# Kernel tuning notes

Hardware: AMD Instinct MI355X
Metric: run time of the kernel (lower is better)

## Reference

```python
import jax, jax.numpy as jnp
import numpy as np

D_MODEL = 1024
NUM_HEADS = 16
D_K = D_MODEL // NUM_HEADS  # 64


def _xavier(key, shape):
    fan_in, fan_out = shape[-1], shape[-2]
    limit = float(np.sqrt(6.0 / (fan_in + fan_out)))
    return jax.random.uniform(key, shape, jnp.float32, -limit, limit)


def setup_inputs() -> dict:
    key = jax.random.key(0)
    kx, kq, kk, kv, ko = jax.random.split(key, 5)
    x = jax.random.normal(kx, (2, 2048, D_MODEL), dtype=jnp.float32)
    q_heads = _xavier(kq, (NUM_HEADS, D_K, D_MODEL))
    k_heads = _xavier(kk, (NUM_HEADS, D_K, D_MODEL))
    v_heads = _xavier(kv, (NUM_HEADS, D_K, D_MODEL))
    output_proj = _xavier(ko, (D_MODEL, NUM_HEADS * D_K))
    return {"x": x, "q_heads": q_heads, "k_heads": k_heads,
            "v_heads": v_heads, "output_proj": output_proj}


def reference(x, q_heads, k_heads, v_heads, output_proj):
    # x: [b, s, d]; q/k/v_heads: [h, dk, d]; output_proj: [d, h*dk]
    b, s, d = x.shape
    h, dk, _ = q_heads.shape
    scale = 1.0 / jnp.sqrt(jnp.asarray(dk, x.dtype))
    # per-head projections: [b, h, s, dk]
    Q = jnp.einsum('bsd,hkd->bhsk', x, q_heads)
    K = jnp.einsum('bsd,hkd->bhsk', x, k_heads)
    V = jnp.einsum('bsd,hkd->bhsk', x, v_heads)
    scores = jnp.einsum('bhqk,bhsk->bhqs', Q, K) * scale  # [b,h,s,s]
    causal = jnp.tril(jnp.ones((s, s), dtype=bool))       # True where allowed
    scores = jnp.where(causal, scores, -jnp.inf)
    attn = jax.nn.softmax(scores, axis=-1)
    out = jnp.einsum('bhqs,bhsk->bhqk', attn, V)           # [b,h,s,dk]
    out = out.transpose(0, 2, 1, 3).reshape(b, s, h * dk)  # [b,s,h*dk]
    return jnp.einsum('bsk,dk->bsd', out, output_proj)
```

## Files before the change

### kernel.cpp

```cpp
#include <hip/hip_runtime.h>
#include <hip/hip_bf16.h>
#include <math.h>

#define D_MODEL 1024
#define NHEADS  16
#define DK      64
#define SEQ     2048
#define KDIM    1024

typedef __bf16 bf16x8 __attribute__((ext_vector_type(8)));
typedef float  f32x4  __attribute__((ext_vector_type(4)));

__device__ __forceinline__ void gload16(const void* g, void* l) {
    __builtin_amdgcn_global_load_lds(
        (const __attribute__((address_space(1))) void*)g,
        (__attribute__((address_space(3))) void*)l, 16, 0, 0);
}

__device__ __forceinline__ unsigned short f2bf(float f) {
    __hip_bfloat16 h = __float2bfloat16(f);
    return *(unsigned short*)&h;
}

__device__ __forceinline__ unsigned pk2bf(float a, float b) {
    __hip_bfloat162 h = __float22bfloat162_rn(make_float2(a, b));
    return *(unsigned*)&h;
}

#define QSCALE 0.18033688011112042f

__global__ __launch_bounds__(256) void cast_kernel(
    const float* __restrict__ x,
    const float* __restrict__ qw,
    const float* __restrict__ kw,
    const float* __restrict__ vw,
    const float* __restrict__ wo,
    unsigned short* __restrict__ xb,
    unsigned short* __restrict__ wqkv,
    unsigned short* __restrict__ wob)
{
    const size_t t = (size_t)blockIdx.x * 256 + threadIdx.x;
    const size_t X4 = 1048576;
    const size_t W4 = 262144;

    const float* src;
    unsigned short* dst;
    size_t o;
    if (t < X4)            { src = x;  dst = xb;             o = t; }
    else if (t < X4 + W4)  { src = qw; dst = wqkv;           o = t - X4; }
    else if (t < X4 + 2*W4){ src = kw; dst = wqkv + 1048576; o = t - X4 - W4; }
    else if (t < X4 + 3*W4){ src = vw; dst = wqkv + 2097152; o = t - X4 - 2*W4; }
    else                   { src = wo; dst = wob;            o = t - X4 - 3*W4; }

    float4 v = ((const float4*)src)[o];
    ushort4 r;
    r.x = f2bf(v.x); r.y = f2bf(v.y); r.z = f2bf(v.z); r.w = f2bf(v.w);
    ((ushort4*)dst)[o] = r;
}

template<int MODE>
__global__ __launch_bounds__(256) void mfma_gemm(
    const unsigned short* __restrict__ A,
    const unsigned short* __restrict__ B,
    float* __restrict__ C0,
    unsigned short* __restrict__ Qb,
    unsigned short* __restrict__ Kb,
    unsigned short* __restrict__ Vtb)
{
    __shared__ __align__(16) unsigned short smem[16384];
    unsigned short* As = smem;
    unsigned short* Bs = smem + 4096;

    const int tid  = threadIdx.x;
    const int wave = tid >> 6;
    const int lane = tid & 63;
    const int wr   = wave >> 1;
    const int wc   = wave & 1;
    const int quad = lane >> 4;
    const int l16  = lane & 15;

    const int rowBase = blockIdx.y * 128;
    const int colBase = blockIdx.x * 128;

    f32x4 acc[4][4];
    const f32x4 z = {0.f, 0.f, 0.f, 0.f};
#pragma unroll
    for (int i = 0; i < 4; ++i)
#pragma unroll
        for (int j = 0; j < 4; ++j) acc[i][j] = z;

    const int srow = lane >> 2;
    const int skof = (lane & 3) * 8;

    for (int k0 = 0; k0 < KDIM; k0 += 32) {
        __syncthreads();

        const unsigned short* ga =
            A + (size_t)(rowBase + wave * 32) * KDIM + k0;
        gload16(ga + (size_t)srow * KDIM + skof,        &As[(wave*32)    * 32]);
        gload16(ga + (size_t)(16 + srow) * KDIM + skof, &As[(wave*32+16) * 32]);

        const unsigned short* gb =
            B + (size_t)(colBase + wave * 32) * KDIM + k0;
        gload16(gb + (size_t)srow * KDIM + skof,        &Bs[(wave*32)    * 32]);
        gload16(gb + (size_t)(16 + srow) * KDIM + skof, &Bs[(wave*32+16) * 32]);

        __syncthreads();

        bf16x8 af[4], bfr[4];
#pragma unroll
        for (int t = 0; t < 4; ++t)
            af[t] = *(const bf16x8*)&As[(wr*64 + t*16 + l16) * 32 + quad*8];
#pragma unroll
        for (int t = 0; t < 4; ++t)
            bfr[t] = *(const bf16x8*)&Bs[(wc*64 + t*16 + l16) * 32 + quad*8];

#pragma unroll
        for (int tr = 0; tr < 4; ++tr)
#pragma unroll
            for (int tc = 0; tc < 4; ++tc)
                acc[tr][tc] = __builtin_amdgcn_mfma_f32_16x16x32_bf16(
                    af[tr], bfr[tc], acc[tr][tc], 0, 0, 0);
    }

    if (MODE == 0) {
        const int mat = colBase >> 10;
        const int b   = rowBase >> 11;
        const int sblk = rowBase & (SEQ - 1);
        if (mat == 2) {
#pragma unroll
            for (int tr = 0; tr < 4; ++tr) {
#pragma unroll
                for (int tc = 0; tc < 4; ++tc) {
                    const int s0 = sblk + wr*64 + tr*16 + quad*4;
                    const int kk = (colBase & 1023) + wc*64 + tc*16 + l16;
                    const int h  = kk >> 6, dk = kk & 63;
                    ushort4 pk;
                    pk.x = f2bf(acc[tr][tc][0]); pk.y = f2bf(acc[tr][tc][1]);
                    pk.z = f2bf(acc[tr][tc][2]); pk.w = f2bf(acc[tr][tc][3]);
                    *(ushort4*)(Vtb + ((size_t)(b*NHEADS + h)*DK + dk)*SEQ + s0) = pk;
                }
            }
        } else {
            const float sc = (mat == 0) ? QSCALE : 1.0f;
            __syncthreads();
#pragma unroll
            for (int tr = 0; tr < 4; ++tr) {
#pragma unroll
                for (int tc = 0; tc < 4; ++tc) {
                    const int col   = wc*64 + tc*16 + l16;
                    const int cbase = col >> 3, c7 = col & 7;
#pragma unroll
                    for (int reg = 0; reg < 4; ++reg) {
                        const int row = wr*64 + tr*16 + quad*4 + reg;
                        const int chunk = cbase ^ (row & 15);
                        smem[row*128 + chunk*8 + c7] = f2bf(acc[tr][tc][reg] * sc);
                    }
                }
            }
            __syncthreads();
            const int h0 = (colBase & 1023) >> 6;
            unsigned short* dstb = (mat == 0) ? Qb : Kb;
#pragma unroll
            for (int i = 0; i < 8; ++i) {
                const int g    = i*256 + tid;
                const int head = g >> 10;
                const int s    = (g >> 3) & 127;
                const int ci   = g & 7;
                const int chunk = (head*8 + ci) ^ (s & 15);
                uint4 v = *(uint4*)&smem[s*128 + chunk*8];
                *(uint4*)(dstb + ((size_t)(b*NHEADS + h0 + head)*SEQ + sblk + s)*DK
                               + ci*8) = v;
            }
        }
    } else {
#pragma unroll
        for (int tr = 0; tr < 4; ++tr) {
#pragma unroll
            for (int tc = 0; tc < 4; ++tc) {
                const int grow0 = rowBase + wr*64 + tr*16 + quad*4;
                const int gcol  = colBase + wc*64 + tc*16 + l16;
#pragma unroll
                for (int reg = 0; reg < 4; ++reg)
                    C0[(size_t)(grow0 + reg) * D_MODEL + gcol] = acc[tr][tc][reg];
            }
        }
    }
}

__global__ __launch_bounds__(256) void attn_mfma_kernel(
    const unsigned short* __restrict__ Qb,
    const unsigned short* __restrict__ Kb,
    const unsigned short* __restrict__ Vtb,
    unsigned short* __restrict__ O)
{
    __shared__ unsigned short Ks[64 * 64];
    __shared__ unsigned short Vs[64 * 64];
    __shared__ unsigned short Ps[4 * 16 * 64];

    const int bh   = blockIdx.x;
    const int qt   = 31 - blockIdx.y;
    const int wave = threadIdx.x >> 6;
    const int lane = threadIdx.x & 63;
    const int quad = lane >> 4;
    const int l16  = lane & 15;

    const size_t qrow = (size_t)bh * SEQ + qt*64 + wave*16 + l16;
    bf16x8 aq0 = *(const bf16x8*)(Qb + qrow * DK + quad*8);
    bf16x8 aq1 = *(const bf16x8*)(Qb + qrow * DK + 32 + quad*8);

    f32x4 o_acc[4];
    const f32x4 z = {0.f, 0.f, 0.f, 0.f};
#pragma unroll
    for (int i = 0; i < 4; ++i) o_acc[i] = z;
    float lrow = 0.f;

    const int srow8  = lane >> 3;
    const int schunk = lane & 7;
    const unsigned short* Kbase = Kb  + (size_t)bh * SEQ * DK;
    const unsigned short* Vbase = Vtb + (size_t)bh * DK * SEQ;
    unsigned short* Pw = &Ps[wave * 1024];

    const int ntiles = qt + 1;
    for (int jt = 0; jt < ntiles; ++jt) {
        const int j0 = jt * 64;
        __syncthreads();
#pragma unroll
        for (int n = 0; n < 2; ++n) {
            const int r = wave*16 + n*8 + srow8;
            gload16(Kbase + (size_t)(j0 + r) * DK + (schunk ^ srow8) * 8,
                    &Ks[(wave*16 + n*8) * 64]);
            gload16(Vbase + (size_t)r * SEQ + j0 + (schunk ^ srow8) * 8,
                    &Vs[(wave*16 + n*8) * 64]);
        }
        __syncthreads();

        f32x4 st[4];
#pragma unroll
        for (int ct = 0; ct < 4; ++ct) {
            const int r = ct*16 + l16;
            bf16x8 k0 = *(const bf16x8*)&Ks[r*64 + ((quad     ^ (r&7)) * 8)];
            bf16x8 k1 = *(const bf16x8*)&Ks[r*64 + (((4+quad) ^ (r&7)) * 8)];
            f32x4 t = z;
            t = __builtin_amdgcn_mfma_f32_16x16x32_bf16(k0, aq0, t, 0, 0, 0);
            t = __builtin_amdgcn_mfma_f32_16x16x32_bf16(k1, aq1, t, 0, 0, 0);
            st[ct] = t;
        }

        if (jt == qt) {
#pragma unroll
            for (int ct = 0; ct < 4; ++ct)
#pragma unroll
                for (int reg = 0; reg < 4; ++reg) {
                    const int kl = ct*16 + quad*4 + reg;
                    const int ql = wave*16 + l16;
                    if (kl > ql) st[ct][reg] = -1e30f;
                }
        }

        float rs = 0.f;
#pragma unroll
        for (int ct = 0; ct < 4; ++ct)
#pragma unroll
            for (int reg = 0; reg < 4; ++reg) {
                float p = exp2f(st[ct][reg]);
                st[ct][reg] = p;
                rs += p;
            }
        rs += __shfl_xor(rs, 16);
        rs += __shfl_xor(rs, 32);
        lrow += rs;

#pragma unroll
        for (int ct = 0; ct < 4; ++ct) {
            uint2 pk;
            pk.x = pk2bf(st[ct][0], st[ct][1]);
            pk.y = pk2bf(st[ct][2], st[ct][3]);
            const int g = (ct*4 + quad) ^ ((l16 & 7) << 1);
            *(uint2*)(Pw + l16*64 + g*4) = pk;
        }

        bf16x8 bp0 = *(const bf16x8*)(Pw + l16*64 + ((quad     ^ (l16&7)) * 8));
        bf16x8 bp1 = *(const bf16x8*)(Pw + l16*64 + (((4+quad) ^ (l16&7)) * 8));

#pragma unroll
        for (int ot = 0; ot < 4; ++ot) {
            const int r = ot*16 + l16;
            bf16x8 v0 = *(const bf16x8*)&Vs[r*64 + ((quad     ^ (r&7)) * 8)];
            bf16x8 v1 = *(const bf16x8*)&Vs[r*64 + (((4+quad) ^ (r&7)) * 8)];
            o_acc[ot] = __builtin_amdgcn_mfma_f32_16x16x32_bf16(v0, bp0, o_acc[ot], 0, 0, 0);
            o_acc[ot] = __builtin_amdgcn_mfma_f32_16x16x32_bf16(v1, bp1, o_acc[ot], 0, 0, 0);
        }
    }

    const float inv = 1.f / lrow;
    const int b = bh >> 4, h = bh & 15;
    const int sg = qt*64 + wave*16 + l16;
    unsigned short* orow = O + ((size_t)(b * SEQ + sg)) * D_MODEL + h * DK;
#pragma unroll
    for (int ot = 0; ot < 4; ++ot) {
        uint2 pk;
        pk.x = pk2bf(o_acc[ot][0] * inv, o_acc[ot][1] * inv);
        pk.y = pk2bf(o_acc[ot][2] * inv, o_acc[ot][3] * inv);
        *(uint2*)(orow + ot*16 + quad*4) = pk;
    }
}

extern "C" void kernel_launch(void* const* d_in, const int* in_sizes, int n_in,
                              void* d_out, int out_size, void* d_ws, size_t ws_size,
                              hipStream_t stream) {
    const float* x  = (const float*)d_in[0];
    const float* qw = (const float*)d_in[1];
    const float* kw = (const float*)d_in[2];
    const float* vw = (const float*)d_in[3];
    const float* wo = (const float*)d_in[4];
    float* out = (float*)d_out;

    char* ws = (char*)d_ws;
    unsigned short* Qb   = (unsigned short*)(ws);
    unsigned short* Kb   = (unsigned short*)(ws + (size_t) 8*1024*1024);
    unsigned short* Vtb  = (unsigned short*)(ws + (size_t)16*1024*1024);
    unsigned short* AO   = (unsigned short*)(ws + (size_t)24*1024*1024);
    unsigned short* XB   = (unsigned short*)(ws + (size_t)32*1024*1024);
    unsigned short* WQKV = (unsigned short*)(ws + (size_t)40*1024*1024);
    unsigned short* WOB  = (unsigned short*)(ws + (size_t)46*1024*1024);

    cast_kernel<<<8192, 256, 0, stream>>>(x, qw, kw, vw, wo, XB, WQKV, WOB);

    dim3 g1(24, 32);
    mfma_gemm<0><<<g1, 256, 0, stream>>>(XB, WQKV, nullptr, Qb, Kb, Vtb);

    dim3 g2(32, 32);
    attn_mfma_kernel<<<g2, 256, 0, stream>>>(Qb, Kb, Vtb, AO);

    dim3 g3(8, 32);
    mfma_gemm<1><<<g3, 256, 0, stream>>>(AO, WOB, out, nullptr, nullptr, nullptr);
}
```

Baseline: 187.5 us.

## Feed P to PV MFMA from registers and retile output projection GEMM

In the attention kernel, the softmax probabilities are no longer staged through per-wave shared memory. They are packed straight into register fragments for the 16x16x16 bf16 MFMA variant, with V read in matching 4-element chunks. This removes LDS writes and reads of P, but doubles the MFMA instruction count and adds more, smaller V loads. Separately, the output projection moves to its own GEMM kernel with 64x128 tiles, doubling the grid to 512 blocks for better CU occupancy on a small GEMM.

```diff
diff --git a/kernel.cpp b/kernel.cpp
--- a/kernel.cpp
+++ b/kernel.cpp
@@ -9,6 +9,7 @@
 #define KDIM    1024
 
 typedef __bf16 bf16x8 __attribute__((ext_vector_type(8)));
+typedef short  s16x4  __attribute__((ext_vector_type(4)));
 typedef float  f32x4  __attribute__((ext_vector_type(4)));
 
 __device__ __forceinline__ void gload16(const void* g, void* l) {
@@ -58,11 +59,9 @@
     ((ushort4*)dst)[o] = r;
 }
 
-template<int MODE>
-__global__ __launch_bounds__(256) void mfma_gemm(
+__global__ __launch_bounds__(256) void mfma_gemm_qkv(
     const unsigned short* __restrict__ A,
     const unsigned short* __restrict__ B,
-    float* __restrict__ C0,
     unsigned short* __restrict__ Qb,
     unsigned short* __restrict__ Kb,
     unsigned short* __restrict__ Vtb)
@@ -123,67 +122,53 @@
                     af[tr], bfr[tc], acc[tr][tc], 0, 0, 0);
     }
 
-    if (MODE == 0) {
-        const int mat = colBase >> 10;
-        const int b   = rowBase >> 11;
-        const int sblk = rowBase & (SEQ - 1);
-        if (mat == 2) {
-#pragma unroll
-            for (int tr = 0; tr < 4; ++tr) {
-#pragma unroll
-                for (int tc = 0; tc < 4; ++tc) {
-                    const int s0 = sblk + wr*64 + tr*16 + quad*4;
-                    const int kk = (colBase & 1023) + wc*64 + tc*16 + l16;
-                    const int h  = kk >> 6, dk = kk & 63;
-                    ushort4 pk;
-                    pk.x = f2bf(acc[tr][tc][0]); pk.y = f2bf(acc[tr][tc][1]);
-                    pk.z = f2bf(acc[tr][tc][2]); pk.w = f2bf(acc[tr][tc][3]);
-                    *(ushort4*)(Vtb + ((size_t)(b*NHEADS + h)*DK + dk)*SEQ + s0) = pk;
+    const int mat = colBase >> 10;
+    const int b   = rowBase >> 11;
+    const int sblk = rowBase & (SEQ - 1);
+    if (mat == 2) {
+#pragma unroll
+        for (int tr = 0; tr < 4; ++tr) {
+#pragma unroll
+            for (int tc = 0; tc < 4; ++tc) {
+                const int s0 = sblk + wr*64 + tr*16 + quad*4;
+                const int kk = (colBase & 1023) + wc*64 + tc*16 + l16;
+                const int h  = kk >> 6, dk = kk & 63;
+                ushort4 pk;
+                pk.x = f2bf(acc[tr][tc][0]); pk.y = f2bf(acc[tr][tc][1]);
+                pk.z = f2bf(acc[tr][tc][2]); pk.w = f2bf(acc[tr][tc][3]);
+                *(ushort4*)(Vtb + ((size_t)(b*NHEADS + h)*DK + dk)*SEQ + s0) = pk;
+            }
+        }
+    } else {
+        const float sc = (mat == 0) ? QSCALE : 1.0f;
+        __syncthreads();
+#pragma unroll
+        for (int tr = 0; tr < 4; ++tr) {
+#pragma unroll
+            for (int tc = 0; tc < 4; ++tc) {
+                const int col   = wc*64 + tc*16 + l16;
+                const int cbase = col >> 3, c7 = col & 7;
+#pragma unroll
+                for (int reg = 0; reg < 4; ++reg) {
+                    const int row = wr*64 + tr*16 + quad*4 + reg;
+                    const int chunk = cbase ^ (row & 15);
+                    smem[row*128 + chunk*8 + c7] = f2bf(acc[tr][tc][reg] * sc);
                 }
             }
-        } else {
-            const float sc = (mat == 0) ? QSCALE : 1.0f;
-            __syncthreads();
-#pragma unroll
-            for (int tr = 0; tr < 4; ++tr) {
-#pragma unroll
-                for (int tc = 0; tc < 4; ++tc) {
-                    const int col   = wc*64 + tc*16 + l16;
-                    const int cbase = col >> 3, c7 = col & 7;
-#pragma unroll
-                    for (int reg = 0; reg < 4; ++reg) {
-                        const int row = wr*64 + tr*16 + quad*4 + reg;
-                        const int chunk = cbase ^ (row & 15);
-                        smem[row*128 + chunk*8 + c7] = f2bf(acc[tr][tc][reg] * sc);
-                    }
-                }
-            }
-            __syncthreads();
-            const int h0 = (colBase & 1023) >> 6;
-            unsigned short* dstb = (mat == 0) ? Qb : Kb;
-#pragma unroll
-            for (int i = 0; i < 8; ++i) {
-                const int g    = i*256 + tid;
-                const int head = g >> 10;
-                const int s    = (g >> 3) & 127;
-                const int ci   = g & 7;
-                const int chunk = (head*8 + ci) ^ (s & 15);
-                uint4 v = *(uint4*)&smem[s*128 + chunk*8];
-                *(uint4*)(dstb + ((size_t)(b*NHEADS + h0 + head)*SEQ + sblk + s)*DK
-                               + ci*8) = v;
-            }
-        }
-    } else {
-#pragma unroll
-        for (int tr = 0; tr < 4; ++tr) {
-#pragma unroll
-            for (int tc = 0; tc < 4; ++tc) {
-                const int grow0 = rowBase + wr*64 + tr*16 + quad*4;
-                const int gcol  = colBase + wc*64 + tc*16 + l16;
-#pragma unroll
-                for (int reg = 0; reg < 4; ++reg)
-                    C0[(size_t)(grow0 + reg) * D_MODEL + gcol] = acc[tr][tc][reg];
-            }
+        }
+        __syncthreads();
+        const int h0 = (colBase & 1023) >> 6;
+        unsigned short* dstb = (mat == 0) ? Qb : Kb;
+#pragma unroll
+        for (int i = 0; i < 8; ++i) {
+            const int g    = i*256 + tid;
+            const int head = g >> 10;
+            const int s    = (g >> 3) & 127;
+            const int ci   = g & 7;
+            const int chunk = (head*8 + ci) ^ (s & 15);
+            uint4 v = *(uint4*)&smem[s*128 + chunk*8];
+            *(uint4*)(dstb + ((size_t)(b*NHEADS + h0 + head)*SEQ + sblk + s)*DK
+                           + ci*8) = v;
         }
     }
 }
@@ -196,7 +181,6 @@
 {
     __shared__ unsigned short Ks[64 * 64];
     __shared__ unsigned short Vs[64 * 64];
-    __shared__ unsigned short Ps[4 * 16 * 64];
 
     const int bh   = blockIdx.x;
     const int qt   = 31 - blockIdx.y;
@@ -219,7 +203,6 @@
     const int schunk = lane & 7;
     const unsigned short* Kbase = Kb  + (size_t)bh * SEQ * DK;
     const unsigned short* Vbase = Vtb + (size_t)bh * DK * SEQ;
-    unsigned short* Pw = &Ps[wave * 1024];
 
     const int ntiles = qt + 1;
     for (int jt = 0; jt < ntiles; ++jt) {
@@ -271,25 +254,26 @@
         rs += __shfl_xor(rs, 32);
         lrow += rs;
 
+        s16x4 pf[4];
 #pragma unroll
         for (int ct = 0; ct < 4; ++ct) {
-            uint2 pk;
-            pk.x = pk2bf(st[ct][0], st[ct][1]);
-            pk.y = pk2bf(st[ct][2], st[ct][3]);
-            const int g = (ct*4 + quad) ^ ((l16 & 7) << 1);
-            *(uint2*)(Pw + l16*64 + g*4) = pk;
-        }
-
-        bf16x8 bp0 = *(const bf16x8*)(Pw + l16*64 + ((quad     ^ (l16&7)) * 8));
-        bf16x8 bp1 = *(const bf16x8*)(Pw + l16*64 + (((4+quad) ^ (l16&7)) * 8));
+            union { unsigned u[2]; s16x4 s; } cv;
+            cv.u[0] = pk2bf(st[ct][0], st[ct][1]);
+            cv.u[1] = pk2bf(st[ct][2], st[ct][3]);
+            pf[ct] = cv.s;
+        }
 
 #pragma unroll
         for (int ot = 0; ot < 4; ++ot) {
             const int r = ot*16 + l16;
-            bf16x8 v0 = *(const bf16x8*)&Vs[r*64 + ((quad     ^ (r&7)) * 8)];
-            bf16x8 v1 = *(const bf16x8*)&Vs[r*64 + (((4+quad) ^ (r&7)) * 8)];
-            o_acc[ot] = __builtin_amdgcn_mfma_f32_16x16x32_bf16(v0, bp0, o_acc[ot], 0, 0, 0);
-            o_acc[ot] = __builtin_amdgcn_mfma_f32_16x16x32_bf16(v1, bp1, o_acc[ot], 0, 0, 0);
+#pragma unroll
+            for (int ct = 0; ct < 4; ++ct) {
+                const int cix = ct*2 + (quad >> 1);
+                s16x4 vf = *(const s16x4*)&Vs[r*64 + ((cix ^ (r&7)) << 3)
+                                              + (quad & 1) * 4];
+                o_acc[ot] = __builtin_amdgcn_mfma_f32_16x16x16bf16_1k(
+                    vf, pf[ct], o_acc[ot], 0, 0, 0);
+            }
         }
     }
 
@@ -303,6 +287,78 @@
         pk.x = pk2bf(o_acc[ot][0] * inv, o_acc[ot][1] * inv);
         pk.y = pk2bf(o_acc[ot][2] * inv, o_acc[ot][3] * inv);
         *(uint2*)(orow + ot*16 + quad*4) = pk;
+    }
+}
+
+__global__ __launch_bounds__(256) void mfma_gemm_out(
+    const unsigned short* __restrict__ A,
+    const unsigned short* __restrict__ B,
+    float* __restrict__ C0)
+{
+    __shared__ __align__(16) unsigned short As[64 * 32];
+    __shared__ __align__(16) unsigned short Bs[128 * 32];
+
+    const int tid  = threadIdx.x;
+    const int wave = tid >> 6;
+    const int lane = tid & 63;
+    const int wr   = wave & 1;
+    const int wc   = wave >> 1;
+    const int quad = lane >> 4;
+    const int l16  = lane & 15;
+
+    const int rowBase = blockIdx.y * 64;
+    const int colBase = blockIdx.x * 128;
+
+    f32x4 acc[2][4];
+    const f32x4 z = {0.f, 0.f, 0.f, 0.f};
+#pragma unroll
+    for (int i = 0; i < 2; ++i)
+#pragma unroll
+        for (int j = 0; j < 4; ++j) acc[i][j] = z;
+
+    const int srow = lane >> 2;
+    const int skof = (lane & 3) * 8;
+
+    for (int k0 = 0; k0 < KDIM; k0 += 32) {
+        __syncthreads();
+
+        const unsigned short* ga =
+            A + (size_t)(rowBase + wave * 16) * KDIM + k0;
+        gload16(ga + (size_t)srow * KDIM + skof, &As[(wave*16) * 32]);
+
+        const unsigned short* gb =
+            B + (size_t)(colBase + wave * 32) * KDIM + k0;
+        gload16(gb + (size_t)srow * KDIM + skof,        &Bs[(wave*32)    * 32]);
+        gload16(gb + (size_t)(16 + srow) * KDIM + skof, &Bs[(wave*32+16) * 32]);
+
+        __syncthreads();
+
+        bf16x8 af[2], bfr[4];
+#pragma unroll
+        for (int t = 0; t < 2; ++t)
+            af[t] = *(const bf16x8*)&As[(wr*32 + t*16 + l16) * 32 + quad*8];
+#pragma unroll
+        for (int t = 0; t < 4; ++t)
+            bfr[t] = *(const bf16x8*)&Bs[(wc*64 + t*16 + l16) * 32 + quad*8];
+
+#pragma unroll
+        for (int tr = 0; tr < 2; ++tr)
+#pragma unroll
+            for (int tc = 0; tc < 4; ++tc)
+                acc[tr][tc] = __builtin_amdgcn_mfma_f32_16x16x32_bf16(
+                    af[tr], bfr[tc], acc[tr][tc], 0, 0, 0);
+    }
+
+#pragma unroll
+    for (int tr = 0; tr < 2; ++tr) {
+#pragma unroll
+        for (int tc = 0; tc < 4; ++tc) {
+            const int grow0 = rowBase + wr*32 + tr*16 + quad*4;
+            const int gcol  = colBase + wc*64 + tc*16 + l16;
+#pragma unroll
+            for (int reg = 0; reg < 4; ++reg)
+                C0[(size_t)(grow0 + reg) * D_MODEL + gcol] = acc[tr][tc][reg];
+        }
     }
 }
 
@@ -328,11 +384,11 @@
     cast_kernel<<<8192, 256, 0, stream>>>(x, qw, kw, vw, wo, XB, WQKV, WOB);
 
     dim3 g1(24, 32);
-    mfma_gemm<0><<<g1, 256, 0, stream>>>(XB, WQKV, nullptr, Qb, Kb, Vtb);
+    mfma_gemm_qkv<<<g1, 256, 0, stream>>>(XB, WQKV, Qb, Kb, Vtb);
 
     dim3 g2(32, 32);
     attn_mfma_kernel<<<g2, 256, 0, stream>>>(Qb, Kb, Vtb, AO);
 
-    dim3 g3(8, 32);
-    mfma_gemm<1><<<g3, 256, 0, stream>>>(AO, WOB, out, nullptr, nullptr, nullptr);
-}
+    dim3 g3(8, 64);
+    mfma_gemm_out<<<g3, 256, 0, stream>>>(AO, WOB, out);
+}
```

After: 180.7 us. -3.6%, faster.
